# Optimization experiments

Measured on AMD Instinct MI355X. Metric: run time of the kernel, lower is better.

The kernel has to match this reference:

```python
import jax, jax.numpy as jnp
import numpy as np

B, N, F, H, L = 4, 512, 128, 4, 2
HID = 128            # edge MLP hidden width
LAM = 5.0            # sinkhorn_lambda
ITERS = 10           # sinkhorn_iter
NEG_SLOPE = 0.2      # GAT leaky-relu slope


def setup_inputs() -> dict:
    key = jax.random.key(0)
    ks = jax.random.split(key, 10)
    sc = 0.05
    return {
        "joint_features": jax.random.normal(ks[0], (B, N, F), jnp.float32),
        "joint_coords": jax.random.normal(ks[1], (B, N, 3), jnp.float32),
        # edge MLP: Linear(2F+1 -> 128), Linear(128 -> 1)
        "W1": jax.random.normal(ks[2], (2 * F + 1, HID), jnp.float32) * sc,
        "b1": jnp.zeros((HID,), jnp.float32),
        "W2": jax.random.normal(ks[3], (HID, 1), jnp.float32) * sc,
        "b2": jnp.zeros((1,), jnp.float32),
        # GAT layers (stacked over L): W (F -> H*F), attention vecs a_src/a_dst (H,F), bias (F)
        "Wg": jax.random.normal(ks[4], (L, F, H * F), jnp.float32) * sc,
        "a_src": jax.random.normal(ks[5], (L, H, F), jnp.float32) * sc,
        "a_dst": jax.random.normal(ks[6], (L, H, F), jnp.float32) * sc,
        "bg": jnp.zeros((L, F), jnp.float32),
    }


def _forward(joint_features, joint_coords, W1, b1, W2, b2, Wg, a_src, a_dst, bg):
    Bc, Nc, Fc = joint_features.shape
    # pairwise euclidean distances (B,N,N)  == torch.cdist(p=2)
    diff = joint_coords[:, :, None, :] - joint_coords[:, None, :, :]
    dist = jnp.sqrt(jnp.maximum(jnp.sum(diff * diff, axis=-1), 0.0))
    # edge MLP on cat([feat_i, feat_j, dist]). Fuse the concat by splitting W1
    # into row blocks: [W_a (F,HID); W_b (F,HID); w_d (HID,)] -- same math,
    # avoids materializing the (B,N,N,2F+1) concat tensor.
    Wa, Wb, wd = W1[:Fc], W1[Fc:2 * Fc], W1[2 * Fc]
    ha = joint_features @ Wa                      # (B,N,HID)
    hb = joint_features @ Wb                      # (B,N,HID)
    hidden = jax.nn.relu(ha[:, :, None, :] + hb[:, None, :, :]
                         + dist[..., None] * wd + b1)   # (B,N,N,HID)
    cost = jnp.squeeze(hidden @ W2, -1) + b2[0]         # (B,N,N)
    # Sinkhorn normalization: K = exp(-lambda * C), alternate row/col scaling
    def sink_step(P, _):
        P = P / jnp.sum(P, axis=-1, keepdims=True)
        P = P / jnp.sum(P, axis=-2, keepdims=True)
        return P, None
    adj, _ = jax.lax.scan(sink_step, jnp.exp(-LAM * cost), None, length=ITERS)
    # adj is strictly positive -> to_sparse() yields the fully-connected graph
    # per batch; GATConv(heads=H, concat=False) becomes dense attention over N.
    x = joint_features
    nlayers, nheads = Wg.shape[0], a_src.shape[1]
    for l in range(nlayers):
        xw = (x @ Wg[l]).reshape(Bc, Nc, nheads, Fc)            # (B,N,H,F)
        s_src = jnp.einsum('bnhf,hf->bnh', xw, a_src[l])        # sender score
        s_dst = jnp.einsum('bnhf,hf->bnh', xw, a_dst[l])        # receiver score
        # e[b,i,j,h]: message j -> i
        e = jax.nn.leaky_relu(s_dst[:, :, None, :] + s_src[:, None, :, :], NEG_SLOPE)
        attn = jax.nn.softmax(e, axis=2)                        # softmax over senders j
        x = jnp.einsum('bijh,bjhf->bihf', attn, xw).mean(axis=2) + bg[l]
    final_adj = jax.nn.sigmoid(jnp.einsum('bif,bjf->bij', x, x))
    return final_adj, adj


def reference(joint_features, joint_coords, W1, b1, W2, b2, Wg, a_src, a_dst, bg):
    return _forward(joint_features, joint_coords, W1, b1, W2, b2, Wg, a_src, a_dst, bg)
```

## Files before the change

kernel.cpp:

```cpp
#include <hip/hip_runtime.h>
#include <math.h>

#define NB 4
#define NN 512

__global__ void kA(const float* __restrict__ X, const float* __restrict__ W1,
                   const float* __restrict__ b1, float* __restrict__ ha,
                   float* __restrict__ hb, float* __restrict__ ru) {
  int b = blockIdx.y, n0 = blockIdx.x * 8;
  __shared__ float xs[8][128];
  int t = threadIdx.x;
  for (int q = t; q < 1024; q += 128) {
    int r = q >> 7, f = q & 127;
    xs[r][f] = X[(size_t)(b * NN + n0 + r) * 128 + f];
  }
  int flat = b * 64 + blockIdx.x;
  if (flat < 16) ru[flat * 128 + t] = 0.f;
  __syncthreads();
  float accA[8] = {0,0,0,0,0,0,0,0}, accB[8] = {0,0,0,0,0,0,0,0};
  for (int f = 0; f < 128; ++f) {
    float wa = W1[f * 128 + t];
    float wb = W1[(128 + f) * 128 + t];
#pragma unroll
    for (int r = 0; r < 8; ++r) {
      accA[r] = fmaf(xs[r][f], wa, accA[r]);
      accB[r] = fmaf(xs[r][f], wb, accB[r]);
    }
  }
  float b1v = b1[t];
#pragma unroll
  for (int r = 0; r < 8; ++r) {
    ha[(size_t)(b * NN + n0 + r) * 128 + t] = accA[r] + b1v;
    hb[(size_t)(b * NN + n0 + r) * 128 + t] = accB[r];
  }
}

__global__ void kB(const float* __restrict__ ha, const float* __restrict__ hb,
                   const float* __restrict__ coords, const float* __restrict__ W1,
                   const float* __restrict__ W2, const float* __restrict__ b2,
                   float* __restrict__ Km, float* __restrict__ ru) {
  int b = blockIdx.z, i0 = blockIdx.y * 32, j0 = blockIdx.x * 32;
  __shared__ alignas(16) float As[32][132];
  __shared__ alignas(16) float Bs[32][132];
  __shared__ alignas(16) float wd[128];
  __shared__ alignas(16) float w2[128];
  __shared__ float ci[32][3], cj[32][3];
  int t = threadIdx.x;
  for (int q = t; q < 1024; q += 256) {
    int r = q >> 5, c = (q & 31) * 4;
    *(float4*)&As[r][c] = *(const float4*)&ha[(size_t)(b * NN + i0 + r) * 128 + c];
    *(float4*)&Bs[r][c] = *(const float4*)&hb[(size_t)(b * NN + j0 + r) * 128 + c];
  }
  if (t < 128) { wd[t] = W1[256 * 128 + t]; w2[t] = W2[t]; }
  if (t < 96) ((float*)ci)[t] = coords[(size_t)(b * NN + i0) * 3 + t];
  else if (t < 192) ((float*)cj)[t - 96] = coords[(size_t)(b * NN + j0) * 3 + (t - 96)];
  __syncthreads();
  int tx = t & 15, ty = t >> 4;
  int ia = 2 * ty, ib = ia + 1, ja = tx, jb = tx + 16;
  float d00, d01, d10, d11;
  {
    float ax = ci[ia][0], ay = ci[ia][1], az = ci[ia][2];
    float bx = ci[ib][0], by = ci[ib][1], bz = ci[ib][2];
    float cx0 = cj[ja][0], cy0 = cj[ja][1], cz0 = cj[ja][2];
    float cx1 = cj[jb][0], cy1 = cj[jb][1], cz1 = cj[jb][2];
    float dx, dy, dz;
    dx = ax - cx0; dy = ay - cy0; dz = az - cz0;
    d00 = sqrtf(fmaxf(dx * dx + dy * dy + dz * dz, 0.f));
    dx = ax - cx1; dy = ay - cy1; dz = az - cz1;
    d01 = sqrtf(fmaxf(dx * dx + dy * dy + dz * dz, 0.f));
    dx = bx - cx0; dy = by - cy0; dz = bz - cz0;
    d10 = sqrtf(fmaxf(dx * dx + dy * dy + dz * dz, 0.f));
    dx = bx - cx1; dy = by - cy1; dz = bz - cz1;
    d11 = sqrtf(fmaxf(dx * dx + dy * dy + dz * dz, 0.f));
  }
  float a00 = 0, a01 = 0, a10 = 0, a11 = 0;
  for (int k = 0; k < 128; k += 4) {
    float4 A0 = *(float4*)&As[ia][k];
    float4 A1 = *(float4*)&As[ib][k];
    float4 B0 = *(float4*)&Bs[ja][k];
    float4 B1 = *(float4*)&Bs[jb][k];
    float4 W = *(float4*)&wd[k];
    float4 V = *(float4*)&w2[k];
#pragma unroll
    for (int kk = 0; kk < 4; ++kk) {
      float av = ((float*)&A0)[kk], av1 = ((float*)&A1)[kk];
      float bv = ((float*)&B0)[kk], bv1 = ((float*)&B1)[kk];
      float wv = ((float*)&W)[kk], vv = ((float*)&V)[kk];
      float t00 = fmaxf(fmaf(d00, wv, av + bv), 0.f);
      float t01 = fmaxf(fmaf(d01, wv, av + bv1), 0.f);
      float t10 = fmaxf(fmaf(d10, wv, av1 + bv), 0.f);
      float t11 = fmaxf(fmaf(d11, wv, av1 + bv1), 0.f);
      a00 = fmaf(t00, vv, a00);
      a01 = fmaf(t01, vv, a01);
      a10 = fmaf(t10, vv, a10);
      a11 = fmaf(t11, vv, a11);
    }
  }
  float b2v = b2[0];
  float k00 = __expf(-5.0f * (a00 + b2v));
  float k01 = __expf(-5.0f * (a01 + b2v));
  float k10 = __expf(-5.0f * (a10 + b2v));
  float k11 = __expf(-5.0f * (a11 + b2v));
  size_t r0 = (size_t)(b * NN + i0 + ia) * NN + j0;
  size_t r1 = (size_t)(b * NN + i0 + ib) * NN + j0;
  Km[r0 + ja] = k00; Km[r0 + jb] = k01;
  Km[r1 + ja] = k10; Km[r1 + jb] = k11;
  float s0 = k00 + k01, s1 = k10 + k11;
#pragma unroll
  for (int off = 1; off < 16; off <<= 1) {
    s0 += __shfl_xor(s0, off);
    s1 += __shfl_xor(s1, off);
  }
  if (tx == 0) {
    atomicAdd(&ru[b * NN + i0 + ia], s0);
    atomicAdd(&ru[b * NN + i0 + ib], s1);
  }
}

__global__ __launch_bounds__(512) void kCcol(const float* __restrict__ Km,
                                             const float* __restrict__ ru,
                                             float* __restrict__ rvp) {
  int ic = blockIdx.x, b = blockIdx.y;
  __shared__ float uinv[32];
  int t = threadIdx.x;
  if (t < 32) uinv[t] = 1.0f / ru[b * NN + ic * 32 + t];
  __syncthreads();
  const float* Kp = Km + (size_t)(b * NN + ic * 32) * NN + t;
  float acc = 0.f;
#pragma unroll 8
  for (int ii = 0; ii < 32; ++ii) acc = fmaf(Kp[(size_t)ii * NN], uinv[ii], acc);
  rvp[ic * 2048 + b * NN + t] = acc;
}

__global__ __launch_bounds__(512) void kCrc(const float* __restrict__ Km,
                                            const float* __restrict__ rvpOld,
                                            float* __restrict__ rvpNew,
                                            float* __restrict__ ru) {
  int ic = blockIdx.x, b = blockIdx.y;
  __shared__ float vinv[512];
  __shared__ float uinv[32];
  int t = threadIdx.x;
  {
    float s = 0.f;
#pragma unroll
    for (int q = 0; q < 16; ++q) s += rvpOld[q * 2048 + b * NN + t];
    vinv[t] = 1.0f / s;
  }
  __syncthreads();
  int w = t >> 6, l = t & 63;
#pragma unroll
  for (int m = 0; m < 4; ++m) {
    int r = ic * 32 + w * 4 + m;
    const float* Kp = Km + (size_t)(b * NN + r) * NN;
    float acc = 0.f;
#pragma unroll
    for (int mm = 0; mm < 8; ++mm) acc = fmaf(Kp[l + 64 * mm], vinv[l + 64 * mm], acc);
#pragma unroll
    for (int off = 1; off < 64; off <<= 1) acc += __shfl_xor(acc, off);
    if (l == 0) { uinv[w * 4 + m] = 1.0f / acc; ru[b * NN + r] = acc; }
  }
  __syncthreads();
  {
    const float* Kp = Km + (size_t)(b * NN + ic * 32) * NN + t;
    float acc = 0.f;
#pragma unroll 8
    for (int ii = 0; ii < 32; ++ii) acc = fmaf(Kp[(size_t)ii * NN], uinv[ii], acc);
    rvpNew[ic * 2048 + b * NN + t] = acc;
  }
}

__global__ __launch_bounds__(512) void kAdj(const float* __restrict__ Km,
                                            const float* __restrict__ ru,
                                            const float* __restrict__ rvp,
                                            float* __restrict__ out) {
  int rc = blockIdx.x, b = blockIdx.y;
  __shared__ float vinv[512];
  __shared__ float uinv[32];
  int t = threadIdx.x;
  {
    float s = 0.f;
#pragma unroll
    for (int ic = 0; ic < 16; ++ic) s += rvp[ic * 2048 + b * NN + t];
    vinv[t] = 1.0f / s;
  }
  if (t < 32) uinv[t] = 1.0f / ru[b * NN + rc * 32 + t];
  __syncthreads();
  float vj = vinv[t];
  const float* Kp = Km + (size_t)(b * NN + rc * 32) * NN + t;
  float* op = out + (size_t)(b * NN + rc * 32) * NN + t;
#pragma unroll 4
  for (int m = 0; m < 32; ++m) {
    op[(size_t)m * NN] = Kp[(size_t)m * NN] * uinv[m] * vj;
  }
}

__global__ void kG1f(const float* __restrict__ x, const float* __restrict__ Wg,
                     const float* __restrict__ asrc, const float* __restrict__ adst,
                     float* __restrict__ xw, float* __restrict__ ssT,
                     float* __restrict__ sdT) {
  int b = blockIdx.y, n0 = blockIdx.x * 8;
  __shared__ float xs[8][128];
  __shared__ float red[4][8][4];
  int t = threadIdx.x;
  for (int q = t; q < 1024; q += 256) {
    int r = q >> 7, f = q & 127;
    xs[r][f] = x[(size_t)(b * NN + n0 + r) * 128 + f];
  }
  __syncthreads();
  int c0 = t, c1 = t + 256;
  float acc0[8] = {0,0,0,0,0,0,0,0}, acc1[8] = {0,0,0,0,0,0,0,0};
  for (int f = 0; f < 128; ++f) {
    float w0 = Wg[f * 512 + c0], w1 = Wg[f * 512 + c1];
#pragma unroll
    for (int r = 0; r < 8; ++r) {
      float xv = xs[r][f];
      acc0[r] = fmaf(xv, w0, acc0[r]);
      acc1[r] = fmaf(xv, w1, acc1[r]);
    }
  }
#pragma unroll
  for (int r = 0; r < 8; ++r) {
    xw[(size_t)(b * NN + n0 + r) * 512 + c0] = acc0[r];
    xw[(size_t)(b * NN + n0 + r) * 512 + c1] = acc1[r];
  }
  float as0 = asrc[c0], ad0 = adst[c0];
  float as1 = asrc[c1], ad1 = adst[c1];
  int w = t >> 6, l = t & 63;
#pragma unroll
  for (int r = 0; r < 8; ++r) {
    float ps0 = acc0[r] * as0, pd0 = acc0[r] * ad0;
    float ps1 = acc1[r] * as1, pd1 = acc1[r] * ad1;
#pragma unroll
    for (int off = 1; off < 64; off <<= 1) {
      ps0 += __shfl_xor(ps0, off);
      pd0 += __shfl_xor(pd0, off);
      ps1 += __shfl_xor(ps1, off);
      pd1 += __shfl_xor(pd1, off);
    }
    if (l == 0) {
      red[w][r][0] = ps0; red[w][r][1] = pd0;
      red[w][r][2] = ps1; red[w][r][3] = pd1;
    }
  }
  __syncthreads();
  if (t < 64) {
    int r = t & 7, h = (t >> 3) & 3, sd = t >> 5;
    int wbase = (h & 1) ? 2 : 0;
    int which = (h < 2 ? 0 : 2) + sd;
    float s = red[wbase][r][which] + red[wbase + 1][r][which];
    float* dst = sd ? sdT : ssT;
    dst[(size_t)(b * 4 + h) * 512 + n0 + r] = s;
  }
}

#define PLDV 520
__global__ __launch_bounds__(512) void kG2v(const float* __restrict__ xw,
                                            const float* __restrict__ ssT,
                                            const float* __restrict__ sdT,
                                            const float* __restrict__ bg,
                                            float* __restrict__ xo) {
  int b = blockIdx.y, i0 = blockIdx.x * 8;
  __shared__ alignas(16) float smem[8192];
  __shared__ float ssb[512];
  __shared__ float sdl[4][8];
  __shared__ float smaxsh[8];
  __shared__ float mxl[8];
  int t = threadIdx.x;
  if (t < 32) {
    int h = t >> 3, r = t & 7;
    sdl[h][r] = sdT[(size_t)(b * 4 + h) * 512 + i0 + r];
  }
  int fq = t & 31, jh = t >> 5;
  int il = t >> 6, jq = t & 63;
  float4 acc[8];
#pragma unroll
  for (int r = 0; r < 8; ++r) acc[r] = make_float4(0.f, 0.f, 0.f, 0.f);
  for (int h = 0; h < 4; ++h) {
    __syncthreads();
    {
      float v = ssT[(size_t)(b * 4 + h) * 512 + t];
      ssb[t] = v;
#pragma unroll
      for (int off = 1; off < 64; off <<= 1) v = fmaxf(v, __shfl_xor(v, off));
      if ((t & 63) == 0) smaxsh[t >> 6] = v;
    }
    __syncthreads();
    if (t < 8) {
      float m = smaxsh[0];
#pragma unroll
      for (int q = 1; q < 8; ++q) m = fmaxf(m, smaxsh[q]);
      float mm = sdl[h][t] + m;
      mxl[t] = (mm >= 0.f) ? mm : 0.2f * mm;
    }
    __syncthreads();
    {
      float mx = mxl[il], sdv = sdl[h][il];
      float pe[8];
      float den = 0.f;
#pragma unroll
      for (int jj = 0; jj < 8; ++jj) {
        int j = jj * 64 + jq;
        float e = sdv + ssb[j];
        e = (e >= 0.f) ? e : 0.2f * e;
        pe[jj] = __expf(e - mx);
        den += pe[jj];
      }
#pragma unroll
      for (int off = 1; off < 64; off <<= 1) den += __shfl_xor(den, off);
      float inv = 1.0f / (4.0f * den);
#pragma unroll
      for (int jj = 0; jj < 8; ++jj) smem[il * PLDV + jj * 64 + jq] = pe[jj] * inv;
    }
    __syncthreads();
    const float* xp = xw + (size_t)(b * NN) * 512 + h * 128 + fq * 4;
    int jbase = jh * 32;
#pragma unroll 4
    for (int jj = 0; jj < 32; ++jj) {
      int j = jbase + jj;
      float4 xv = *(const float4*)&xp[(size_t)j * 512];
#pragma unroll
      for (int r = 0; r < 8; ++r) {
        float p = smem[r * PLDV + j];
        acc[r].x = fmaf(p, xv.x, acc[r].x);
        acc[r].y = fmaf(p, xv.y, acc[r].y);
        acc[r].z = fmaf(p, xv.z, acc[r].z);
        acc[r].w = fmaf(p, xv.w, acc[r].w);
      }
    }
  }
  __syncthreads();
  int w = t >> 6;
#pragma unroll
  for (int r = 0; r < 8; ++r) {
    acc[r].x += __shfl_xor(acc[r].x, 32);
    acc[r].y += __shfl_xor(acc[r].y, 32);
    acc[r].z += __shfl_xor(acc[r].z, 32);
    acc[r].w += __shfl_xor(acc[r].w, 32);
  }
  float4* sc4 = (float4*)smem;
  if ((t & 63) < 32) {
#pragma unroll
    for (int r = 0; r < 8; ++r) sc4[w * 256 + r * 32 + fq] = acc[r];
  }
  __syncthreads();
  if (t < 256) {
    int r = t >> 5, ff = t & 31;
    float4 bb = *(const float4*)&bg[ff * 4];
    float4 s = bb;
#pragma unroll
    for (int q = 0; q < 8; ++q) {
      float4 u = sc4[q * 256 + r * 32 + ff];
      s.x += u.x; s.y += u.y; s.z += u.z; s.w += u.w;
    }
    *(float4*)&xo[(size_t)(b * NN + i0 + r) * 128 + ff * 4] = s;
  }
}

__global__ void kF(const float* __restrict__ x, float* __restrict__ out) {
  int b = blockIdx.z, i0 = blockIdx.y * 32, j0 = blockIdx.x * 32;
  __shared__ alignas(16) float As[32][132];
  __shared__ alignas(16) float Bs[32][132];
  int t = threadIdx.x;
  for (int q = t; q < 1024; q += 256) {
    int r = q >> 5, c = (q & 31) * 4;
    *(float4*)&As[r][c] = *(const float4*)&x[(size_t)(b * NN + i0 + r) * 128 + c];
    *(float4*)&Bs[r][c] = *(const float4*)&x[(size_t)(b * NN + j0 + r) * 128 + c];
  }
  __syncthreads();
  int tx = t & 15, ty = t >> 4;
  int ia = 2 * ty, ib = ia + 1, ja = tx, jb = tx + 16;
  float a00 = 0, a01 = 0, a10 = 0, a11 = 0;
  for (int k = 0; k < 128; k += 4) {
    float4 A0 = *(float4*)&As[ia][k];
    float4 A1 = *(float4*)&As[ib][k];
    float4 B0 = *(float4*)&Bs[ja][k];
    float4 B1 = *(float4*)&Bs[jb][k];
#pragma unroll
    for (int kk = 0; kk < 4; ++kk) {
      float av = ((float*)&A0)[kk], av1 = ((float*)&A1)[kk];
      float bv = ((float*)&B0)[kk], bv1 = ((float*)&B1)[kk];
      a00 = fmaf(av, bv, a00);
      a01 = fmaf(av, bv1, a01);
      a10 = fmaf(av1, bv, a10);
      a11 = fmaf(av1, bv1, a11);
    }
  }
  size_t r0 = (size_t)(b * NN + i0 + ia) * NN + j0;
  size_t r1 = (size_t)(b * NN + i0 + ib) * NN + j0;
  out[r0 + ja] = 1.0f / (1.0f + __expf(-a00));
  out[r0 + jb] = 1.0f / (1.0f + __expf(-a01));
  out[r1 + ja] = 1.0f / (1.0f + __expf(-a10));
  out[r1 + jb] = 1.0f / (1.0f + __expf(-a11));
}

extern "C" void kernel_launch(void* const* d_in, const int* in_sizes, int n_in,
                              void* d_out, int out_size, void* d_ws, size_t ws_size,
                              hipStream_t stream) {
  (void)in_sizes; (void)n_in; (void)out_size; (void)ws_size;
  const float* X   = (const float*)d_in[0];
  const float* C   = (const float*)d_in[1];
  const float* W1  = (const float*)d_in[2];
  const float* b1  = (const float*)d_in[3];
  const float* W2  = (const float*)d_in[4];
  const float* b2  = (const float*)d_in[5];
  const float* Wg  = (const float*)d_in[6];
  const float* as_ = (const float*)d_in[7];
  const float* ad_ = (const float*)d_in[8];
  const float* bg  = (const float*)d_in[9];
  float* out = (float*)d_out;
  float* ws = (float*)d_ws;

  float* ha    = ws;
  float* hb    = ws + 262144;
  float* Km    = ws + 524288;
  float* ru    = ws + 1572864;
  float* xw    = ws + 1591296;
  float* ssT   = ws + 2639872;
  float* sdT   = ws + 2648064;
  float* x1    = ws + 2656256;
  float* x2    = ws + 2918400;
  float* rvpA  = ws + 3180544;
  float* rvpB  = ws + 3246080;
  float* adj   = out + 1048576;

  kA<<<dim3(64, 4), 128, 0, stream>>>(X, W1, b1, ha, hb, ru);
  kB<<<dim3(16, 16, 4), 256, 0, stream>>>(ha, hb, C, W1, W2, b2, Km, ru);
  kCcol<<<dim3(16, 4), 512, 0, stream>>>(Km, ru, rvpA);
  for (int it = 0; it < 9; ++it) {
    const float* src = (it & 1) ? rvpB : rvpA;
    float* dst = (it & 1) ? rvpA : rvpB;
    kCrc<<<dim3(16, 4), 512, 0, stream>>>(Km, src, dst, ru);
  }
  kAdj<<<dim3(16, 4), 512, 0, stream>>>(Km, ru, rvpB, adj);
  kG1f<<<dim3(64, 4), 256, 0, stream>>>(X, Wg, as_, ad_, xw, ssT, sdT);
  kG2v<<<dim3(64, 4), 512, 0, stream>>>(xw, ssT, sdT, bg, x1);
  kG1f<<<dim3(64, 4), 256, 0, stream>>>(x1, Wg + 65536, as_ + 512, ad_ + 512, xw, ssT, sdT);
  kG2v<<<dim3(64, 4), 512, 0, stream>>>(xw, ssT, sdT, bg + 128, x2);
  kF<<<dim3(16, 16, 4), 256, 0, stream>>>(x2, out);
}
```

Measured before the change: 189.2 us.

## Co-schedule Sinkhorn iterations with independent GAT stages in combined launches

Merges the small 64-block Sinkhorn row/column kernels with the independent GAT projection, attention, and final outer-product kernels into shared launches. The first 16 blocks in x run a Sinkhorn step and the rest run the GAT work. The intent is to fill the otherwise idle GPU during the latency-bound Sinkhorn chain and to cut the number of launches. The combined kernels take the larger of the two shared-memory footprints and 512 threads, so the GAT kernels are rewritten for 512 threads and occupancy may drop.

```diff
diff --git a/kernel.cpp b/kernel.cpp
--- a/kernel.cpp
+++ b/kernel.cpp
@@ -117,11 +117,12 @@
   }
 }
 
-__global__ __launch_bounds__(512) void kCcol(const float* __restrict__ Km,
-                                             const float* __restrict__ ru,
-                                             float* __restrict__ rvp) {
-  int ic = blockIdx.x, b = blockIdx.y;
-  __shared__ float uinv[32];
+
+__device__ __forceinline__ void dCcol(const float* __restrict__ Km,
+                                      const float* __restrict__ ru,
+                                      float* __restrict__ rvp,
+                                      float* sm, int ic, int b) {
+  float* uinv = sm;
   int t = threadIdx.x;
   if (t < 32) uinv[t] = 1.0f / ru[b * NN + ic * 32 + t];
   __syncthreads();
@@ -132,13 +133,13 @@
   rvp[ic * 2048 + b * NN + t] = acc;
 }
 
-__global__ __launch_bounds__(512) void kCrc(const float* __restrict__ Km,
-                                            const float* __restrict__ rvpOld,
-                                            float* __restrict__ rvpNew,
-                                            float* __restrict__ ru) {
-  int ic = blockIdx.x, b = blockIdx.y;
-  __shared__ float vinv[512];
-  __shared__ float uinv[32];
+__device__ __forceinline__ void dCrc(const float* __restrict__ Km,
+                                     const float* __restrict__ rvpOld,
+                                     float* __restrict__ rvpNew,
+                                     float* __restrict__ ru,
+                                     float* sm, int ic, int b) {
+  float* vinv = sm;
+  float* uinv = sm + 512;
   int t = threadIdx.x;
   {
     float s = 0.f;
@@ -167,6 +168,228 @@
     for (int ii = 0; ii < 32; ++ii) acc = fmaf(Kp[(size_t)ii * NN], uinv[ii], acc);
     rvpNew[ic * 2048 + b * NN + t] = acc;
   }
+}
+
+__device__ __forceinline__ void dG1f(const float* __restrict__ x,
+                                     const float* __restrict__ Wg,
+                                     const float* __restrict__ asrc,
+                                     const float* __restrict__ adst,
+                                     float* __restrict__ xw,
+                                     float* __restrict__ ssT,
+                                     float* __restrict__ sdT,
+                                     float* sm, int bx, int b) {
+  int n0 = bx * 8;
+  float* xs = sm;
+  float* red = sm + 1024;
+  int t = threadIdx.x;
+  for (int q = t; q < 1024; q += 512)
+    xs[q] = x[(size_t)(b * NN + n0 + (q >> 7)) * 128 + (q & 127)];
+  __syncthreads();
+  int c = t;
+  float acc[8] = {0,0,0,0,0,0,0,0};
+  for (int f = 0; f < 128; ++f) {
+    float w0 = Wg[f * 512 + c];
+#pragma unroll
+    for (int r = 0; r < 8; ++r) acc[r] = fmaf(xs[r * 128 + f], w0, acc[r]);
+  }
+#pragma unroll
+  for (int r = 0; r < 8; ++r)
+    xw[(size_t)(b * NN + n0 + r) * 512 + c] = acc[r];
+  float asv = asrc[c], adv = adst[c];
+  int w = t >> 6, l = t & 63;
+#pragma unroll
+  for (int r = 0; r < 8; ++r) {
+    float ps = acc[r] * asv, pd = acc[r] * adv;
+#pragma unroll
+    for (int off = 1; off < 64; off <<= 1) {
+      ps += __shfl_xor(ps, off);
+      pd += __shfl_xor(pd, off);
+    }
+    if (l == 0) { red[w * 16 + r * 2] = ps; red[w * 16 + r * 2 + 1] = pd; }
+  }
+  __syncthreads();
+  if (t < 64) {
+    int h = t >> 4, rr = t & 7, sd = (t >> 3) & 1;
+    float s = red[(2 * h) * 16 + rr * 2 + sd] + red[(2 * h + 1) * 16 + rr * 2 + sd];
+    float* dst = sd ? sdT : ssT;
+    dst[(size_t)(b * 4 + h) * 512 + n0 + rr] = s;
+  }
+}
+
+#define PLDV 520
+__device__ __forceinline__ void dG2v(const float* __restrict__ xw,
+                                     const float* __restrict__ ssT,
+                                     const float* __restrict__ sdT,
+                                     const float* __restrict__ bg,
+                                     float* __restrict__ xo,
+                                     float* sm, int bx, int b) {
+  int i0 = bx * 8;
+  float* pls = sm;
+  float* ssb = sm + 8192;
+  float* sdl = sm + 8704;
+  float* smaxsh = sm + 8736;
+  float* mxl = sm + 8744;
+  int t = threadIdx.x;
+  if (t < 32) {
+    int h = t >> 3, r = t & 7;
+    sdl[h * 8 + r] = sdT[(size_t)(b * 4 + h) * 512 + i0 + r];
+  }
+  int fq = t & 31, jh = t >> 5;
+  int il = t >> 6, jq = t & 63;
+  float4 acc[8];
+#pragma unroll
+  for (int r = 0; r < 8; ++r) acc[r] = make_float4(0.f, 0.f, 0.f, 0.f);
+  for (int h = 0; h < 4; ++h) {
+    __syncthreads();
+    {
+      float v = ssT[(size_t)(b * 4 + h) * 512 + t];
+      ssb[t] = v;
+#pragma unroll
+      for (int off = 1; off < 64; off <<= 1) v = fmaxf(v, __shfl_xor(v, off));
+      if ((t & 63) == 0) smaxsh[t >> 6] = v;
+    }
+    __syncthreads();
+    if (t < 8) {
+      float m = smaxsh[0];
+#pragma unroll
+      for (int q = 1; q < 8; ++q) m = fmaxf(m, smaxsh[q]);
+      float mm = sdl[h * 8 + t] + m;
+      mxl[t] = (mm >= 0.f) ? mm : 0.2f * mm;
+    }
+    __syncthreads();
+    {
+      float mx = mxl[il], sdv = sdl[h * 8 + il];
+      float pe[8];
+      float den = 0.f;
+#pragma unroll
+      for (int jj = 0; jj < 8; ++jj) {
+        int j = jj * 64 + jq;
+        float e = sdv + ssb[j];
+        e = (e >= 0.f) ? e : 0.2f * e;
+        pe[jj] = __expf(e - mx);
+        den += pe[jj];
+      }
+#pragma unroll
+      for (int off = 1; off < 64; off <<= 1) den += __shfl_xor(den, off);
+      float inv = 1.0f / (4.0f * den);
+#pragma unroll
+      for (int jj = 0; jj < 8; ++jj) pls[il * PLDV + jj * 64 + jq] = pe[jj] * inv;
+    }
+    __syncthreads();
+    const float* xp = xw + (size_t)(b * NN) * 512 + h * 128 + fq * 4;
+    int jbase = jh * 32;
+#pragma unroll 4
+    for (int jj = 0; jj < 32; ++jj) {
+      int j = jbase + jj;
+      float4 xv = *(const float4*)&xp[(size_t)j * 512];
+#pragma unroll
+      for (int r = 0; r < 8; ++r) {
+        float p = pls[r * PLDV + j];
+        acc[r].x = fmaf(p, xv.x, acc[r].x);
+        acc[r].y = fmaf(p, xv.y, acc[r].y);
+        acc[r].z = fmaf(p, xv.z, acc[r].z);
+        acc[r].w = fmaf(p, xv.w, acc[r].w);
+      }
+    }
+  }
+  __syncthreads();
+  int w = t >> 6;
+#pragma unroll
+  for (int r = 0; r < 8; ++r) {
+    acc[r].x += __shfl_xor(acc[r].x, 32);
+    acc[r].y += __shfl_xor(acc[r].y, 32);
+    acc[r].z += __shfl_xor(acc[r].z, 32);
+    acc[r].w += __shfl_xor(acc[r].w, 32);
+  }
+  float4* sc4 = (float4*)pls;
+  if ((t & 63) < 32) {
+#pragma unroll
+    for (int r = 0; r < 8; ++r) sc4[w * 256 + r * 32 + fq] = acc[r];
+  }
+  __syncthreads();
+  if (t < 256) {
+    int r = t >> 5, ff = t & 31;
+    float4 bb = *(const float4*)&bg[ff * 4];
+    float4 s = bb;
+#pragma unroll
+    for (int q = 0; q < 8; ++q) {
+      float4 u = sc4[q * 256 + r * 32 + ff];
+      s.x += u.x; s.y += u.y; s.z += u.z; s.w += u.w;
+    }
+    *(float4*)&xo[(size_t)(b * NN + i0 + r) * 128 + ff * 4] = s;
+  }
+}
+
+__device__ __forceinline__ void dF(const float* __restrict__ x,
+                                   float* __restrict__ out,
+                                   float* sm, int fid, int b) {
+  int i0 = (fid >> 4) * 32, j0 = (fid & 15) * 32;
+  float* As = sm;
+  float* Bs = sm + 4224;
+  int t = threadIdx.x;
+  for (int q = t; q < 1024; q += 512) {
+    int r = q >> 5, c = (q & 31) * 4;
+    *(float4*)&As[r * 132 + c] = *(const float4*)&x[(size_t)(b * NN + i0 + r) * 128 + c];
+    *(float4*)&Bs[r * 132 + c] = *(const float4*)&x[(size_t)(b * NN + j0 + r) * 128 + c];
+  }
+  __syncthreads();
+  int tx = t & 31, ty = t >> 5;
+  int ia = 2 * ty, ib = ia + 1;
+  float a0 = 0.f, a1 = 0.f;
+  for (int k = 0; k < 128; k += 4) {
+    float4 A0 = *(float4*)&As[ia * 132 + k];
+    float4 A1 = *(float4*)&As[ib * 132 + k];
+    float4 B0 = *(float4*)&Bs[tx * 132 + k];
+#pragma unroll
+    for (int kk = 0; kk < 4; ++kk) {
+      a0 = fmaf(((float*)&A0)[kk], ((float*)&B0)[kk], a0);
+      a1 = fmaf(((float*)&A1)[kk], ((float*)&B0)[kk], a1);
+    }
+  }
+  out[(size_t)(b * NN + i0 + ia) * NN + j0 + tx] = 1.0f / (1.0f + __expf(-a0));
+  out[(size_t)(b * NN + i0 + ib) * NN + j0 + tx] = 1.0f / (1.0f + __expf(-a1));
+}
+
+
+__global__ __launch_bounds__(512) void nCcolG1f(
+    const float* Km, const float* ru, float* rvpA,
+    const float* X, const float* Wg, const float* as_, const float* ad_,
+    float* xw, float* ssT, float* sdT) {
+  __shared__ alignas(16) float sm[1280];
+  if (blockIdx.x < 16) dCcol(Km, ru, rvpA, sm, blockIdx.x, blockIdx.y);
+  else dG1f(X, Wg, as_, ad_, xw, ssT, sdT, sm, blockIdx.x - 16, blockIdx.y);
+}
+
+__global__ __launch_bounds__(512) void nCrcG2v(
+    const float* Km, const float* rvpOld, float* rvpNew, float* ru,
+    const float* xw, const float* ssT, const float* sdT,
+    const float* bg, float* xo) {
+  __shared__ alignas(16) float sm[8752];
+  if (blockIdx.x < 16) dCrc(Km, rvpOld, rvpNew, ru, sm, blockIdx.x, blockIdx.y);
+  else dG2v(xw, ssT, sdT, bg, xo, sm, blockIdx.x - 16, blockIdx.y);
+}
+
+__global__ __launch_bounds__(512) void nCrcG1f(
+    const float* Km, const float* rvpOld, float* rvpNew, float* ru,
+    const float* x, const float* Wg, const float* as_, const float* ad_,
+    float* xw, float* ssT, float* sdT) {
+  __shared__ alignas(16) float sm[1280];
+  if (blockIdx.x < 16) dCrc(Km, rvpOld, rvpNew, ru, sm, blockIdx.x, blockIdx.y);
+  else dG1f(x, Wg, as_, ad_, xw, ssT, sdT, sm, blockIdx.x - 16, blockIdx.y);
+}
+
+__global__ __launch_bounds__(512) void nCrcF(
+    const float* Km, const float* rvpOld, float* rvpNew, float* ru,
+    const float* x, float* outF) {
+  __shared__ alignas(16) float sm[8448];
+  if (blockIdx.x < 16) dCrc(Km, rvpOld, rvpNew, ru, sm, blockIdx.x, blockIdx.y);
+  else dF(x, outF, sm, blockIdx.x - 16, blockIdx.y);
+}
+
+__global__ __launch_bounds__(512) void kCrc(
+    const float* Km, const float* rvpOld, float* rvpNew, float* ru) {
+  __shared__ alignas(16) float sm[544];
+  dCrc(Km, rvpOld, rvpNew, ru, sm, blockIdx.x, blockIdx.y);
 }
 
 __global__ __launch_bounds__(512) void kAdj(const float* __restrict__ Km,
@@ -192,205 +415,6 @@
   for (int m = 0; m < 32; ++m) {
     op[(size_t)m * NN] = Kp[(size_t)m * NN] * uinv[m] * vj;
   }
-}
-
-__global__ void kG1f(const float* __restrict__ x, const float* __restrict__ Wg,
-                     const float* __restrict__ asrc, const float* __restrict__ adst,
-                     float* __restrict__ xw, float* __restrict__ ssT,
-                     float* __restrict__ sdT) {
-  int b = blockIdx.y, n0 = blockIdx.x * 8;
-  __shared__ float xs[8][128];
-  __shared__ float red[4][8][4];
-  int t = threadIdx.x;
-  for (int q = t; q < 1024; q += 256) {
-    int r = q >> 7, f = q & 127;
-    xs[r][f] = x[(size_t)(b * NN + n0 + r) * 128 + f];
-  }
-  __syncthreads();
-  int c0 = t, c1 = t + 256;
-  float acc0[8] = {0,0,0,0,0,0,0,0}, acc1[8] = {0,0,0,0,0,0,0,0};
-  for (int f = 0; f < 128; ++f) {
-    float w0 = Wg[f * 512 + c0], w1 = Wg[f * 512 + c1];
-#pragma unroll
-    for (int r = 0; r < 8; ++r) {
-      float xv = xs[r][f];
-      acc0[r] = fmaf(xv, w0, acc0[r]);
-      acc1[r] = fmaf(xv, w1, acc1[r]);
-    }
-  }
-#pragma unroll
-  for (int r = 0; r < 8; ++r) {
-    xw[(size_t)(b * NN + n0 + r) * 512 + c0] = acc0[r];
-    xw[(size_t)(b * NN + n0 + r) * 512 + c1] = acc1[r];
-  }
-  float as0 = asrc[c0], ad0 = adst[c0];
-  float as1 = asrc[c1], ad1 = adst[c1];
-  int w = t >> 6, l = t & 63;
-#pragma unroll
-  for (int r = 0; r < 8; ++r) {
-    float ps0 = acc0[r] * as0, pd0 = acc0[r] * ad0;
-    float ps1 = acc1[r] * as1, pd1 = acc1[r] * ad1;
-#pragma unroll
-    for (int off = 1; off < 64; off <<= 1) {
-      ps0 += __shfl_xor(ps0, off);
-      pd0 += __shfl_xor(pd0, off);
-      ps1 += __shfl_xor(ps1, off);
-      pd1 += __shfl_xor(pd1, off);
-    }
-    if (l == 0) {
-      red[w][r][0] = ps0; red[w][r][1] = pd0;
-      red[w][r][2] = ps1; red[w][r][3] = pd1;
-    }
-  }
-  __syncthreads();
-  if (t < 64) {
-    int r = t & 7, h = (t >> 3) & 3, sd = t >> 5;
-    int wbase = (h & 1) ? 2 : 0;
-    int which = (h < 2 ? 0 : 2) + sd;
-    float s = red[wbase][r][which] + red[wbase + 1][r][which];
-    float* dst = sd ? sdT : ssT;
-    dst[(size_t)(b * 4 + h) * 512 + n0 + r] = s;
-  }
-}
-
-#define PLDV 520
-__global__ __launch_bounds__(512) void kG2v(const float* __restrict__ xw,
-                                            const float* __restrict__ ssT,
-                                            const float* __restrict__ sdT,
-                                            const float* __restrict__ bg,
-                                            float* __restrict__ xo) {
-  int b = blockIdx.y, i0 = blockIdx.x * 8;
-  __shared__ alignas(16) float smem[8192];
-  __shared__ float ssb[512];
-  __shared__ float sdl[4][8];
-  __shared__ float smaxsh[8];
-  __shared__ float mxl[8];
-  int t = threadIdx.x;
-  if (t < 32) {
-    int h = t >> 3, r = t & 7;
-    sdl[h][r] = sdT[(size_t)(b * 4 + h) * 512 + i0 + r];
-  }
-  int fq = t & 31, jh = t >> 5;
-  int il = t >> 6, jq = t & 63;
-  float4 acc[8];
-#pragma unroll
-  for (int r = 0; r < 8; ++r) acc[r] = make_float4(0.f, 0.f, 0.f, 0.f);
-  for (int h = 0; h < 4; ++h) {
-    __syncthreads();
-    {
-      float v = ssT[(size_t)(b * 4 + h) * 512 + t];
-      ssb[t] = v;
-#pragma unroll
-      for (int off = 1; off < 64; off <<= 1) v = fmaxf(v, __shfl_xor(v, off));
-      if ((t & 63) == 0) smaxsh[t >> 6] = v;
-    }
-    __syncthreads();
-    if (t < 8) {
-      float m = smaxsh[0];
-#pragma unroll
-      for (int q = 1; q < 8; ++q) m = fmaxf(m, smaxsh[q]);
-      float mm = sdl[h][t] + m;
-      mxl[t] = (mm >= 0.f) ? mm : 0.2f * mm;
-    }
-    __syncthreads();
-    {
-      float mx = mxl[il], sdv = sdl[h][il];
-      float pe[8];
-      float den = 0.f;
-#pragma unroll
-      for (int jj = 0; jj < 8; ++jj) {
-        int j = jj * 64 + jq;
-        float e = sdv + ssb[j];
-        e = (e >= 0.f) ? e : 0.2f * e;
-        pe[jj] = __expf(e - mx);
-        den += pe[jj];
-      }
-#pragma unroll
-      for (int off = 1; off < 64; off <<= 1) den += __shfl_xor(den, off);
-      float inv = 1.0f / (4.0f * den);
-#pragma unroll
-      for (int jj = 0; jj < 8; ++jj) smem[il * PLDV + jj * 64 + jq] = pe[jj] * inv;
-    }
-    __syncthreads();
-    const float* xp = xw + (size_t)(b * NN) * 512 + h * 128 + fq * 4;
-    int jbase = jh * 32;
-#pragma unroll 4
-    for (int jj = 0; jj < 32; ++jj) {
-      int j = jbase + jj;
-      float4 xv = *(const float4*)&xp[(size_t)j * 512];
-#pragma unroll
-      for (int r = 0; r < 8; ++r) {
-        float p = smem[r * PLDV + j];
-        acc[r].x = fmaf(p, xv.x, acc[r].x);
-        acc[r].y = fmaf(p, xv.y, acc[r].y);
-        acc[r].z = fmaf(p, xv.z, acc[r].z);
-        acc[r].w = fmaf(p, xv.w, acc[r].w);
-      }
-    }
-  }
-  __syncthreads();
-  int w = t >> 6;
-#pragma unroll
-  for (int r = 0; r < 8; ++r) {
-    acc[r].x += __shfl_xor(acc[r].x, 32);
-    acc[r].y += __shfl_xor(acc[r].y, 32);
-    acc[r].z += __shfl_xor(acc[r].z, 32);
-    acc[r].w += __shfl_xor(acc[r].w, 32);
-  }
-  float4* sc4 = (float4*)smem;
-  if ((t & 63) < 32) {
-#pragma unroll
-    for (int r = 0; r < 8; ++r) sc4[w * 256 + r * 32 + fq] = acc[r];
-  }
-  __syncthreads();
-  if (t < 256) {
-    int r = t >> 5, ff = t & 31;
-    float4 bb = *(const float4*)&bg[ff * 4];
-    float4 s = bb;
-#pragma unroll
-    for (int q = 0; q < 8; ++q) {
-      float4 u = sc4[q * 256 + r * 32 + ff];
-      s.x += u.x; s.y += u.y; s.z += u.z; s.w += u.w;
-    }
-    *(float4*)&xo[(size_t)(b * NN + i0 + r) * 128 + ff * 4] = s;
-  }
-}
-
-__global__ void kF(const float* __restrict__ x, float* __restrict__ out) {
-  int b = blockIdx.z, i0 = blockIdx.y * 32, j0 = blockIdx.x * 32;
-  __shared__ alignas(16) float As[32][132];
-  __shared__ alignas(16) float Bs[32][132];
-  int t = threadIdx.x;
-  for (int q = t; q < 1024; q += 256) {
-    int r = q >> 5, c = (q & 31) * 4;
-    *(float4*)&As[r][c] = *(const float4*)&x[(size_t)(b * NN + i0 + r) * 128 + c];
-    *(float4*)&Bs[r][c] = *(const float4*)&x[(size_t)(b * NN + j0 + r) * 128 + c];
-  }
-  __syncthreads();
-  int tx = t & 15, ty = t >> 4;
-  int ia = 2 * ty, ib = ia + 1, ja = tx, jb = tx + 16;
-  float a00 = 0, a01 = 0, a10 = 0, a11 = 0;
-  for (int k = 0; k < 128; k += 4) {
-    float4 A0 = *(float4*)&As[ia][k];
-    float4 A1 = *(float4*)&As[ib][k];
-    float4 B0 = *(float4*)&Bs[ja][k];
-    float4 B1 = *(float4*)&Bs[jb][k];
-#pragma unroll
-    for (int kk = 0; kk < 4; ++kk) {
-      float av = ((float*)&A0)[kk], av1 = ((float*)&A1)[kk];
-      float bv = ((float*)&B0)[kk], bv1 = ((float*)&B1)[kk];
-      a00 = fmaf(av, bv, a00);
-      a01 = fmaf(av, bv1, a01);
-      a10 = fmaf(av1, bv, a10);
-      a11 = fmaf(av1, bv1, a11);
-    }
-  }
-  size_t r0 = (size_t)(b * NN + i0 + ia) * NN + j0;
-  size_t r1 = (size_t)(b * NN + i0 + ib) * NN + j0;
-  out[r0 + ja] = 1.0f / (1.0f + __expf(-a00));
-  out[r0 + jb] = 1.0f / (1.0f + __expf(-a01));
-  out[r1 + ja] = 1.0f / (1.0f + __expf(-a10));
-  out[r1 + jb] = 1.0f / (1.0f + __expf(-a11));
 }
 
 extern "C" void kernel_launch(void* const* d_in, const int* in_sizes, int n_in,
@@ -425,16 +449,20 @@
 
   kA<<<dim3(64, 4), 128, 0, stream>>>(X, W1, b1, ha, hb, ru);
   kB<<<dim3(16, 16, 4), 256, 0, stream>>>(ha, hb, C, W1, W2, b2, Km, ru);
-  kCcol<<<dim3(16, 4), 512, 0, stream>>>(Km, ru, rvpA);
-  for (int it = 0; it < 9; ++it) {
-    const float* src = (it & 1) ? rvpB : rvpA;
-    float* dst = (it & 1) ? rvpA : rvpB;
-    kCrc<<<dim3(16, 4), 512, 0, stream>>>(Km, src, dst, ru);
-  }
+  nCcolG1f<<<dim3(80, 4), 512, 0, stream>>>(Km, ru, rvpA,
+                                            X, Wg, as_, ad_, xw, ssT, sdT);
+  nCrcG2v<<<dim3(80, 4), 512, 0, stream>>>(Km, rvpA, rvpB, ru,
+                                           xw, ssT, sdT, bg, x1);
+  nCrcG1f<<<dim3(80, 4), 512, 0, stream>>>(Km, rvpB, rvpA, ru,
+                                           x1, Wg + 65536, as_ + 512, ad_ + 512,
+                                           xw, ssT, sdT);
+  nCrcG2v<<<dim3(80, 4), 512, 0, stream>>>(Km, rvpA, rvpB, ru,
+                                           xw, ssT, sdT, bg + 128, x2);
+  nCrcF<<<dim3(272, 4), 512, 0, stream>>>(Km, rvpB, rvpA, ru, x2, out);
+  kCrc<<<dim3(16, 4), 512, 0, stream>>>(Km, rvpA, rvpB, ru);
+  kCrc<<<dim3(16, 4), 512, 0, stream>>>(Km, rvpB, rvpA, ru);
+  kCrc<<<dim3(16, 4), 512, 0, stream>>>(Km, rvpA, rvpB, ru);
+  kCrc<<<dim3(16, 4), 512, 0, stream>>>(Km, rvpB, rvpA, ru);
+  kCrc<<<dim3(16, 4), 512, 0, stream>>>(Km, rvpA, rvpB, ru);
   kAdj<<<dim3(16, 4), 512, 0, stream>>>(Km, ru, rvpB, adj);
-  kG1f<<<dim3(64, 4), 256, 0, stream>>>(X, Wg, as_, ad_, xw, ssT, sdT);
-  kG2v<<<dim3(64, 4), 512, 0, stream>>>(xw, ssT, sdT, bg, x1);
-  kG1f<<<dim3(64, 4), 256, 0, stream>>>(x1, Wg + 65536, as_ + 512, ad_ + 512, xw, ssT, sdT);
-  kG2v<<<dim3(64, 4), 512, 0, stream>>>(xw, ssT, sdT, bg + 128, x2);
-  kF<<<dim3(16, 16, 4), 256, 0, stream>>>(x2, out);
-}
+}
```

New measurement: 177.8 us. 1.06x faster.
